# Optimization experiments

Hardware: AMD Instinct MI355X
Metric: run time of the kernel (lower is better)

Reference implementation:

```python
import jax, jax.numpy as jnp
import numpy as np

B, C, H, W = 16, 256, 64, 64
HEADS = 8


def setup_inputs() -> dict:
    key = jax.random.key(0)
    ks = jax.random.split(key, 12)
    s = 0.02
    return {
        "x": jax.random.normal(ks[0], (B, C, H, W), jnp.float32),
        "Wq": jax.random.normal(ks[1], (C, C), jnp.float32) * s,
        "bq": jnp.zeros((C,), jnp.float32),
        "Wk": jax.random.normal(ks[2], (C, C), jnp.float32) * s,
        "bk": jnp.zeros((C,), jnp.float32),
        "Wv": jax.random.normal(ks[3], (C, C), jnp.float32) * s,
        "bv": jnp.zeros((C,), jnp.float32),
        "gamma": jax.random.normal(ks[4], (1,), jnp.float32) * 0.5,
        "beta": jax.random.normal(ks[5], (1,), jnp.float32) * 0.5,
        "W1": jax.random.normal(ks[6], (C, C), jnp.float32) * s,
        "b1": jnp.zeros((C,), jnp.float32),
        "u1": jax.random.normal(ks[7], (C,), jnp.float32),
        "W2": jax.random.normal(ks[8], (C, C), jnp.float32) * s,
        "b2": jnp.zeros((C,), jnp.float32),
        "u2": jax.random.normal(ks[9], (C,), jnp.float32),
    }


def _conv1x1(x, Wt, b):
    # 1x1 conv == per-pixel GEMM over channels
    return jnp.einsum('oc,bchw->bohw', Wt, x) + b[None, :, None, None]


def _l2(v):
    return v / (jnp.linalg.norm(v) + 1e-12)


def _spectral_norm(Wt, u):
    # one power iteration (torch SpectralNorm wrapper), u treated as buffer
    Wm = Wt.reshape(Wt.shape[0], -1)
    v = _l2(Wm.T @ u)
    u_new = _l2(Wm @ v)
    sigma = u_new @ (Wm @ v)
    return Wt / sigma


def reference(x, Wq, bq, Wk, bk, Wv, bv, gamma, beta, W1, b1, u1, W2, b2, u2):
    Bn, Cn, Hh, Ww = x.shape
    N = Hh * Ww
    d = Cn // HEADS
    scale = HEADS ** (-0.5)
    # 1x1 conv projections, then b (h n) s layout -> (B, heads, d, N)
    q = _conv1x1(x, Wq, bq).reshape(Bn, HEADS, d, N)
    k = _conv1x1(x, Wk, bk).reshape(Bn, HEADS, d, N)
    v = _conv1x1(x, Wv, bv).reshape(Bn, HEADS, d, N)
    # per-head channel attention: energy is (B, heads, d, d)
    energy = jnp.einsum('bhis,bhjs->bhij', q, k) * scale
    attn = jax.nn.softmax(energy, axis=-1)
    out = jnp.einsum('bhij,bhjs->bhis', attn, v).reshape(Bn, Cn, Hh, Ww)
    out = gamma * out + x
    # residual refinement net (dropout = identity in eval mode)
    y = _conv1x1(out, _spectral_norm(W1, u1), b1)
    y = jax.nn.leaky_relu(y, 0.1)
    y = _conv1x1(y, _spectral_norm(W2, u2), b2)
    out = out + beta * y
    return (out, attn)
```

## Files before the change

kernel.cpp:

```cpp
#include <hip/hip_runtime.h>
#include <hip/hip_bf16.h>
#include <cstdint>
#include <cstddef>

typedef __attribute__((ext_vector_type(8))) __bf16 bf16x8;
typedef __attribute__((ext_vector_type(4))) float f32x4;
typedef __attribute__((ext_vector_type(8))) unsigned short us8;
typedef __attribute__((ext_vector_type(4))) unsigned short us4;

__device__ __forceinline__ unsigned short f2bf(float f){
  unsigned int u = __float_as_uint(f);
  u += 0x7fffu + ((u >> 16) & 1u);
  return (unsigned short)(u >> 16);
}
__device__ __forceinline__ float bf2f(unsigned short h){
  return __uint_as_float(((unsigned int)h) << 16);
}
__device__ __forceinline__ bf16x8 ldbf8(const unsigned short* p){
  return __builtin_bit_cast(bf16x8, *(const us8*)p);
}
__device__ __forceinline__ void split16(const float* __restrict__ g,
                                        unsigned short* __restrict__ hs,
                                        unsigned short* __restrict__ ls){
  #pragma unroll
  for (int q = 0; q < 4; ++q){
    float4 v = *(const float4*)(g + q*4);
    unsigned short h0=f2bf(v.x), h1=f2bf(v.y), h2=f2bf(v.z), h3=f2bf(v.w);
    us4 hv = {h0,h1,h2,h3};
    us4 lv = { f2bf(v.x - bf2f(h0)), f2bf(v.y - bf2f(h1)),
               f2bf(v.z - bf2f(h2)), f2bf(v.w - bf2f(h3)) };
    *(us4*)(hs + q*4) = hv;
    *(us4*)(ls + q*4) = lv;
  }
}

#define SCALE_E 0.35355339059327373f

static const size_t OFF_XHI    = 0;
static const size_t OFF_XLO    = 33554432;
static const size_t OFF_XTHI   = 67108864;
static const size_t OFF_GPART  = 100663296;
static const size_t OFF_G      = 113246208;
static const size_t OFF_M      = 117440512;
static const size_t OFF_W1S    = 119537664;
static const size_t OFF_W2S    = 119668736;
static const size_t OFF_SIG    = 119799808;
static const size_t OFF_XSUM   = 119799824;
static const size_t OFF_ROWADD = 119816208;

__global__ void k_zero(float* __restrict__ xsum){
  xsum[blockIdx.x * 256 + threadIdx.x] = 0.f;
}

__global__ void k_sigma(const float* __restrict__ W1, const float* __restrict__ u1,
                        const float* __restrict__ W2, const float* __restrict__ u2,
                        float* __restrict__ sig){
  const float* W = blockIdx.x ? W2 : W1;
  const float* u = blockIdx.x ? u2 : u1;
  int t = threadIdx.x;
  __shared__ __align__(16) float red[256];
  __shared__ __align__(16) float vls[256];
  __shared__ __align__(16) float uls[256];
  uls[t] = u[t];
  __syncthreads();
  float t1 = 0.f;
  for (int o = 0; o < 256; ++o) t1 += W[o*256 + t] * uls[o];
  red[t] = t1 * t1;
  __syncthreads();
  for (int s = 128; s > 0; s >>= 1){ if (t < s) red[t] += red[t+s]; __syncthreads(); }
  float nrm = sqrtf(red[0]);
  vls[t] = t1 / (nrm + 1e-12f);
  __syncthreads();
  float w = 0.f;
  const float4* wr4 = (const float4*)(W + t*256);
  for (int c4 = 0; c4 < 64; ++c4){
    float4 a = wr4[c4];
    float4 v = *(const float4*)&vls[c4*4];
    w += a.x*v.x + a.y*v.y + a.z*v.z + a.w*v.w;
  }
  __syncthreads();
  red[t] = w * w;
  __syncthreads();
  for (int s = 128; s > 0; s >>= 1){ if (t < s) red[t] += red[t+s]; __syncthreads(); }
  if (t == 0){
    float s2 = red[0];
    float sn = sqrtf(s2);
    sig[blockIdx.x] = s2 / (sn + 1e-12f);
  }
}

__global__ void k_wconv(const float* __restrict__ W1, const float* __restrict__ W2,
                        const float* __restrict__ sig,
                        unsigned short* __restrict__ W1s, unsigned short* __restrict__ W2s){
  int sel = blockIdx.x >> 6;
  const float* W = sel ? W2 : W1;
  unsigned short* o = sel ? W2s : W1s;
  float inv = 1.0f / sig[sel];
  int base = (blockIdx.x & 63) * 1024 + threadIdx.x * 4;
  float4 v = *(const float4*)&W[base];
  us4 r = { f2bf(v.x*inv), f2bf(v.y*inv), f2bf(v.z*inv), f2bf(v.w*inv) };
  *(us4*)&o[base] = r;
}

__global__ __launch_bounds__(256) void k_convert(const float* __restrict__ x,
    unsigned short* __restrict__ xhi, unsigned short* __restrict__ xlo,
    unsigned short* __restrict__ xthi, float* __restrict__ xsum){
  int b = blockIdx.z, c0 = blockIdx.y*64, n0 = blockIdx.x*64;
  int t = threadIdx.x, tn = t & 15, tc = t >> 4;
  __shared__ __align__(16) unsigned short hs[64][68];
  __shared__ __align__(16) float ps[64][17];
  #pragma unroll
  for (int rr = 0; rr < 4; ++rr){
    int cl = rr*16 + tc;
    size_t gro = ((size_t)(b*256 + c0 + cl))*4096 + n0 + tn*4;
    float4 v = *(const float4*)&x[gro];
    unsigned short h0=f2bf(v.x), h1=f2bf(v.y), h2=f2bf(v.z), h3=f2bf(v.w);
    us4 hv = {h0,h1,h2,h3};
    us4 lv = { f2bf(v.x - bf2f(h0)), f2bf(v.y - bf2f(h1)),
               f2bf(v.z - bf2f(h2)), f2bf(v.w - bf2f(h3)) };
    *(us4*)&xhi[gro] = hv;
    *(us4*)&xlo[gro] = lv;
    *(us4*)&hs[cl][tn*4] = hv;
    ps[cl][tn] = v.x + v.y + v.z + v.w;
  }
  __syncthreads();
  #pragma unroll
  for (int rr = 0; rr < 4; ++rr){
    int nl = rr*16 + tc;
    int cl4 = tn*4;
    us4 w = { hs[cl4+0][nl], hs[cl4+1][nl], hs[cl4+2][nl], hs[cl4+3][nl] };
    *(us4*)&xthi[((size_t)(b*4096 + n0 + nl))*256 + c0 + cl4] = w;
  }
  if (t < 64){
    float s = 0.f;
    #pragma unroll
    for (int k = 0; k < 16; ++k) s += ps[t][k];
    atomicAdd(&xsum[b*256 + c0 + t], s);
  }
}

__global__ __launch_bounds__(256) void k_gram(const unsigned short* __restrict__ xhi,
    const unsigned short* __restrict__ xlo, float* __restrict__ G, float* __restrict__ Gp){
  int b = blockIdx.z;
  int tr = (blockIdx.y >> 1) * 128, tc = (blockIdx.y & 1) * 128;
  int kc = blockIdx.x * 1024;
  int t = threadIdx.x;
  __shared__ __align__(16) unsigned short Ah[2][128*40], Al[2][128*40],
                                          Bh[2][128*40], Bl[2][128*40];
  f32x4 acc[4][4];
  #pragma unroll
  for (int i = 0; i < 4; ++i)
    #pragma unroll
    for (int j = 0; j < 4; ++j) acc[i][j] = (f32x4){0.f,0.f,0.f,0.f};
  int srow = t >> 1, skh = (t & 1) * 16;
  int l = t & 63, wv = t >> 6;
  int wr = (wv >> 1) * 64, wc = (wv & 1) * 64;
  int lr = l & 15, lg = l >> 4;
  size_t bb = (size_t)b * 256 * 4096;
  const unsigned short* gah = xhi + bb + (size_t)(tr + srow)*4096 + kc + skh;
  const unsigned short* gal = xlo + bb + (size_t)(tr + srow)*4096 + kc + skh;
  const unsigned short* gbh = xhi + bb + (size_t)(tc + srow)*4096 + kc + skh;
  const unsigned short* gbl = xlo + bb + (size_t)(tc + srow)*4096 + kc + skh;
  us8 rah0 = *(const us8*)gah, rah1 = *(const us8*)(gah + 8);
  us8 ral0 = *(const us8*)gal, ral1 = *(const us8*)(gal + 8);
  us8 rbh0 = *(const us8*)gbh, rbh1 = *(const us8*)(gbh + 8);
  us8 rbl0 = *(const us8*)gbl, rbl1 = *(const us8*)(gbl + 8);
  int cur = 0;
  for (int ki = 0; ki < 32; ++ki){
    *(us8*)&Ah[cur][srow*40 + skh]     = rah0;
    *(us8*)&Ah[cur][srow*40 + skh + 8] = rah1;
    *(us8*)&Al[cur][srow*40 + skh]     = ral0;
    *(us8*)&Al[cur][srow*40 + skh + 8] = ral1;
    *(us8*)&Bh[cur][srow*40 + skh]     = rbh0;
    *(us8*)&Bh[cur][srow*40 + skh + 8] = rbh1;
    *(us8*)&Bl[cur][srow*40 + skh]     = rbl0;
    *(us8*)&Bl[cur][srow*40 + skh + 8] = rbl1;
    if (ki < 31){
      int ko = (ki + 1) * 32;
      rah0 = *(const us8*)(gah + ko); rah1 = *(const us8*)(gah + ko + 8);
      ral0 = *(const us8*)(gal + ko); ral1 = *(const us8*)(gal + ko + 8);
      rbh0 = *(const us8*)(gbh + ko); rbh1 = *(const us8*)(gbh + ko + 8);
      rbl0 = *(const us8*)(gbl + ko); rbl1 = *(const us8*)(gbl + ko + 8);
    }
    __syncthreads();
    bf16x8 ah[4], alv[4], bh[4], blv[4];
    #pragma unroll
    for (int i = 0; i < 4; ++i){
      ah[i]  = ldbf8(&Ah[cur][(wr + i*16 + lr)*40 + lg*8]);
      alv[i] = ldbf8(&Al[cur][(wr + i*16 + lr)*40 + lg*8]);
      bh[i]  = ldbf8(&Bh[cur][(wc + i*16 + lr)*40 + lg*8]);
      blv[i] = ldbf8(&Bl[cur][(wc + i*16 + lr)*40 + lg*8]);
    }
    #pragma unroll
    for (int i = 0; i < 4; ++i)
      #pragma unroll
      for (int j = 0; j < 4; ++j){
        acc[i][j] = __builtin_amdgcn_mfma_f32_16x16x32_bf16(ah[i],  bh[j],  acc[i][j], 0,0,0);
        acc[i][j] = __builtin_amdgcn_mfma_f32_16x16x32_bf16(ah[i],  blv[j], acc[i][j], 0,0,0);
        acc[i][j] = __builtin_amdgcn_mfma_f32_16x16x32_bf16(alv[i], bh[j],  acc[i][j], 0,0,0);
      }
    cur ^= 1;
  }
  float* dst = (blockIdx.x == 0) ? (G + (size_t)b*65536)
                                 : (Gp + ((size_t)(blockIdx.x - 1)*16 + b)*65536);
  #pragma unroll
  for (int i = 0; i < 4; ++i)
    #pragma unroll
    for (int j = 0; j < 4; ++j)
      #pragma unroll
      for (int r = 0; r < 4; ++r){
        int row = tr + wr + i*16 + lg*4 + r;
        int col = tc + wc + j*16 + lr;
        dst[row*256 + col] = acc[i][j][r];
      }
}

__global__ void k_gred(const float* __restrict__ G0, const float* __restrict__ Gp,
                       unsigned short* __restrict__ Ghi, unsigned short* __restrict__ Glo){
  size_t idx = ((size_t)blockIdx.x * 256 + threadIdx.x) * 4;
  float4 g  = *(const float4*)&G0[idx];
  float4 p0 = *(const float4*)&Gp[idx];
  float4 p1 = *(const float4*)&Gp[idx + 1048576];
  float4 p2 = *(const float4*)&Gp[idx + 2097152];
  float s0 = g.x + p0.x + p1.x + p2.x;
  float s1 = g.y + p0.y + p1.y + p2.y;
  float s2 = g.z + p0.z + p1.z + p2.z;
  float s3 = g.w + p0.w + p1.w + p2.w;
  unsigned short h0=f2bf(s0), h1=f2bf(s1), h2=f2bf(s2), h3=f2bf(s3);
  us4 hv = {h0,h1,h2,h3};
  us4 lv = { f2bf(s0 - bf2f(h0)), f2bf(s1 - bf2f(h1)),
             f2bf(s2 - bf2f(h2)), f2bf(s3 - bf2f(h3)) };
  *(us4*)&Ghi[idx] = hv;
  *(us4*)&Glo[idx] = lv;
}

__global__ __launch_bounds__(256) void k_qg(const float* __restrict__ Wq,
    const unsigned short* __restrict__ Ghi, const unsigned short* __restrict__ Glo,
    unsigned short* __restrict__ Phi, unsigned short* __restrict__ Plo){
  int b = blockIdx.z;
  int tr = blockIdx.y * 128, tc = blockIdx.x * 128;
  int t = threadIdx.x;
  __shared__ __align__(16) unsigned short Ah[128*40], Al[128*40], Bh[128*40], Bl[128*40];
  f32x4 acc[4][4];
  #pragma unroll
  for (int i = 0; i < 4; ++i)
    #pragma unroll
    for (int j = 0; j < 4; ++j) acc[i][j] = (f32x4){0.f,0.f,0.f,0.f};
  int srow = t >> 1, skh = (t & 1) * 16;
  int l = t & 63, wv = t >> 6;
  int wr = (wv >> 1) * 64, wc = (wv & 1) * 64;
  int lr = l & 15, lg = l >> 4;
  for (int kk = 0; kk < 256; kk += 32){
    __syncthreads();
    split16(Wq + (size_t)(tr + srow)*256 + kk + skh, &Ah[srow*40 + skh], &Al[srow*40 + skh]);
    size_t gb = (size_t)b*65536 + (size_t)(tc + srow)*256 + kk + skh;
    *(us8*)&Bh[srow*40 + skh]     = *(const us8*)&Ghi[gb];
    *(us8*)&Bh[srow*40 + skh + 8] = *(const us8*)&Ghi[gb + 8];
    *(us8*)&Bl[srow*40 + skh]     = *(const us8*)&Glo[gb];
    *(us8*)&Bl[srow*40 + skh + 8] = *(const us8*)&Glo[gb + 8];
    __syncthreads();
    bf16x8 ah[4], alv[4], bh[4], blv[4];
    #pragma unroll
    for (int i = 0; i < 4; ++i){
      ah[i]  = ldbf8(&Ah[(wr + i*16 + lr)*40 + lg*8]);
      alv[i] = ldbf8(&Al[(wr + i*16 + lr)*40 + lg*8]);
      bh[i]  = ldbf8(&Bh[(wc + i*16 + lr)*40 + lg*8]);
      blv[i] = ldbf8(&Bl[(wc + i*16 + lr)*40 + lg*8]);
    }
    #pragma unroll
    for (int i = 0; i < 4; ++i)
      #pragma unroll
      for (int j = 0; j < 4; ++j){
        acc[i][j] = __builtin_amdgcn_mfma_f32_16x16x32_bf16(ah[i],  bh[j],  acc[i][j], 0,0,0);
        acc[i][j] = __builtin_amdgcn_mfma_f32_16x16x32_bf16(ah[i],  blv[j], acc[i][j], 0,0,0);
        acc[i][j] = __builtin_amdgcn_mfma_f32_16x16x32_bf16(alv[i], bh[j],  acc[i][j], 0,0,0);
      }
  }
  #pragma unroll
  for (int i = 0; i < 4; ++i)
    #pragma unroll
    for (int j = 0; j < 4; ++j)
      #pragma unroll
      for (int r = 0; r < 4; ++r){
        int row = tr + wr + i*16 + lg*4 + r;
        int col = tc + wc + j*16 + lr;
        size_t off = (size_t)b*65536 + (size_t)row*256 + col;
        float p = acc[i][j][r];
        unsigned short hp = f2bf(p);
        Phi[off] = hp;
        Plo[off] = f2bf(p - bf2f(hp));
      }
}

__global__ __launch_bounds__(256) void k_e(const unsigned short* __restrict__ Phi,
    const unsigned short* __restrict__ Plo, const float* __restrict__ Wk,
    float* __restrict__ Ef){
  int b = blockIdx.z;
  int tr = blockIdx.y * 128, tc = blockIdx.x * 128;
  int t = threadIdx.x;
  __shared__ __align__(16) unsigned short Ah[128*40], Al[128*40], Bh[128*40], Bl[128*40];
  f32x4 acc[4][4];
  #pragma unroll
  for (int i = 0; i < 4; ++i)
    #pragma unroll
    for (int j = 0; j < 4; ++j) acc[i][j] = (f32x4){0.f,0.f,0.f,0.f};
  int srow = t >> 1, skh = (t & 1) * 16;
  int l = t & 63, wv = t >> 6;
  int wr = (wv >> 1) * 64, wc = (wv & 1) * 64;
  int lr = l & 15, lg = l >> 4;
  for (int kk = 0; kk < 256; kk += 32){
    __syncthreads();
    size_t ga = (size_t)b*65536 + (size_t)(tr + srow)*256 + kk + skh;
    *(us8*)&Ah[srow*40 + skh]     = *(const us8*)&Phi[ga];
    *(us8*)&Ah[srow*40 + skh + 8] = *(const us8*)&Phi[ga + 8];
    *(us8*)&Al[srow*40 + skh]     = *(const us8*)&Plo[ga];
    *(us8*)&Al[srow*40 + skh + 8] = *(const us8*)&Plo[ga + 8];
    split16(Wk + (size_t)(tc + srow)*256 + kk + skh, &Bh[srow*40 + skh], &Bl[srow*40 + skh]);
    __syncthreads();
    bf16x8 ah[4], alv[4], bh[4], blv[4];
    #pragma unroll
    for (int i = 0; i < 4; ++i){
      ah[i]  = ldbf8(&Ah[(wr + i*16 + lr)*40 + lg*8]);
      alv[i] = ldbf8(&Al[(wr + i*16 + lr)*40 + lg*8]);
      bh[i]  = ldbf8(&Bh[(wc + i*16 + lr)*40 + lg*8]);
      blv[i] = ldbf8(&Bl[(wc + i*16 + lr)*40 + lg*8]);
    }
    #pragma unroll
    for (int i = 0; i < 4; ++i)
      #pragma unroll
      for (int j = 0; j < 4; ++j){
        acc[i][j] = __builtin_amdgcn_mfma_f32_16x16x32_bf16(ah[i],  bh[j],  acc[i][j], 0,0,0);
        acc[i][j] = __builtin_amdgcn_mfma_f32_16x16x32_bf16(ah[i],  blv[j], acc[i][j], 0,0,0);
        acc[i][j] = __builtin_amdgcn_mfma_f32_16x16x32_bf16(alv[i], bh[j],  acc[i][j], 0,0,0);
      }
  }
  #pragma unroll
  for (int i = 0; i < 4; ++i)
    #pragma unroll
    for (int j = 0; j < 4; ++j)
      #pragma unroll
      for (int r = 0; r < 4; ++r){
        int row = tr + wr + i*16 + lg*4 + r;
        int col = tc + wc + j*16 + lr;
        Ef[(size_t)b*65536 + (size_t)row*256 + col] = SCALE_E * acc[i][j][r];
      }
}

__global__ __launch_bounds__(256) void k_soft(const float* __restrict__ Ef,
    const float* __restrict__ Wq, const float* __restrict__ bq,
    const float* __restrict__ Wk, const float* __restrict__ bk,
    const float* __restrict__ Wv, const float* __restrict__ bv,
    const float* __restrict__ gptr, const float* __restrict__ xsum,
    unsigned short* __restrict__ Mw, float* __restrict__ rowadd,
    float* __restrict__ attn_out){
  int blk = blockIdx.x, b = blk >> 3, h = blk & 7;
  int t = threadIdx.x;
  int i = t >> 3, j4 = (t & 7) * 4;
  __shared__ __align__(16) float Aw[32][40];
  __shared__ float qsv[32], ksv[32];
  if (t < 64){
    int r = t & 31;
    const float* Wm = (t < 32) ? Wq : Wk;
    const float4* wr4 = (const float4*)(Wm + (size_t)(h*32 + r)*256);
    const float4* xs4 = (const float4*)(xsum + b*256);
    float s = 0.f;
    #pragma unroll
    for (int c4 = 0; c4 < 64; ++c4){
      float4 a = wr4[c4], xv = xs4[c4];
      s += a.x*xv.x + a.y*xv.y + a.z*xv.z + a.w*xv.w;
    }
    if (t < 32) qsv[r] = s; else ksv[r] = s;
  }
  __syncthreads();
  float4 e = *(const float4*)&Ef[(size_t)b*65536 + (size_t)(h*32 + i)*256 + h*32 + j4];
  float bqi = bq[h*32 + i];
  float qb  = qsv[i] + 4096.f * bqi;
  e.x += SCALE_E * (bqi*ksv[j4+0] + bk[h*32+j4+0]*qb);
  e.y += SCALE_E * (bqi*ksv[j4+1] + bk[h*32+j4+1]*qb);
  e.z += SCALE_E * (bqi*ksv[j4+2] + bk[h*32+j4+2]*qb);
  e.w += SCALE_E * (bqi*ksv[j4+3] + bk[h*32+j4+3]*qb);
  float m = fmaxf(fmaxf(e.x, e.y), fmaxf(e.z, e.w));
  m = fmaxf(m, __shfl_xor(m, 1));
  m = fmaxf(m, __shfl_xor(m, 2));
  m = fmaxf(m, __shfl_xor(m, 4));
  float ex0 = expf(e.x - m), ex1 = expf(e.y - m), ex2 = expf(e.z - m), ex3 = expf(e.w - m);
  float s = ex0 + ex1 + ex2 + ex3;
  s += __shfl_xor(s, 1); s += __shfl_xor(s, 2); s += __shfl_xor(s, 4);
  float inv = 1.f / s;
  float4 a4 = { ex0*inv, ex1*inv, ex2*inv, ex3*inv };
  *(float4*)&attn_out[(((size_t)(b*8 + h))*32 + i)*32 + j4] = a4;
  *(float4*)&Aw[i][j4] = a4;
  __syncthreads();
  float gamma = gptr[0];
  float mr[32];
  #pragma unroll
  for (int r = 0; r < 32; ++r) mr[r] = 0.f;
  for (int j = 0; j < 32; ++j){
    float wvv = Wv[(size_t)(h*32 + j)*256 + t];
    #pragma unroll
    for (int r = 0; r < 32; ++r) mr[r] += Aw[r][j] * wvv;
  }
  unsigned short* Mrow = Mw + ((size_t)b*256 + h*32)*256 + t;
  #pragma unroll
  for (int r = 0; r < 32; ++r){
    float diag = (h*32 + r == t) ? 1.f : 0.f;
    Mrow[r*256] = f2bf(gamma * mr[r] + diag);
  }
  if (t < 32){
    float sr = 0.f;
    #pragma unroll
    for (int j = 0; j < 32; ++j) sr += Aw[t][j] * bv[h*32 + j];
    rowadd[b*256 + h*32 + t] = gamma * sr;
  }
}

template<int MODE>
__global__ __launch_bounds__(256) void k_gemm(const unsigned short* __restrict__ Aall,
    const unsigned short* __restrict__ Bmat, const unsigned short* __restrict__ oth,
    const float* __restrict__ rowadd, const float* __restrict__ bias,
    const float* __restrict__ betap,
    unsigned short* __restrict__ outb){
  int b = blockIdx.z;
  int n0 = blockIdx.x * 128, o0 = blockIdx.y * 128;
  int t = threadIdx.x;
  __shared__ __align__(16) unsigned short Als[2][128*40], Bls[2][128*40];
  f32x4 acc[4][4];
  #pragma unroll
  for (int i = 0; i < 4; ++i)
    #pragma unroll
    for (int j = 0; j < 4; ++j) acc[i][j] = (f32x4){0.f,0.f,0.f,0.f};
  const unsigned short* A  = Aall + (size_t)b * 1048576;
  const unsigned short* Bp = (MODE == 0) ? (Bmat + (size_t)b * 65536) : Bmat;
  int srow = t >> 1, skh = (t & 1) * 16;
  int l = t & 63, wv = t >> 6;
  int wr = (wv >> 1) * 64, wc = (wv & 1) * 64;
  int lr = l & 15, lg = l >> 4;
  const unsigned short* ga = A  + (size_t)(n0 + srow)*256 + skh;
  const unsigned short* gb = Bp + (size_t)(o0 + srow)*256 + skh;
  us8 ra0 = *(const us8*)ga, ra1 = *(const us8*)(ga + 8);
  us8 rb0 = *(const us8*)gb, rb1 = *(const us8*)(gb + 8);
  #pragma unroll
  for (int ki = 0; ki < 8; ++ki){
    int cur = ki & 1;
    *(us8*)&Als[cur][srow*40 + skh]     = ra0;
    *(us8*)&Als[cur][srow*40 + skh + 8] = ra1;
    *(us8*)&Bls[cur][srow*40 + skh]     = rb0;
    *(us8*)&Bls[cur][srow*40 + skh + 8] = rb1;
    if (ki < 7){
      int ko = (ki + 1) * 32;
      ra0 = *(const us8*)(ga + ko); ra1 = *(const us8*)(ga + ko + 8);
      rb0 = *(const us8*)(gb + ko); rb1 = *(const us8*)(gb + ko + 8);
    }
    __syncthreads();
    bf16x8 af[4], bfv[4];
    #pragma unroll
    for (int i = 0; i < 4; ++i) af[i]  = ldbf8(&Als[cur][(wr + i*16 + lr)*40 + lg*8]);
    #pragma unroll
    for (int j = 0; j < 4; ++j) bfv[j] = ldbf8(&Bls[cur][(wc + j*16 + lr)*40 + lg*8]);
    #pragma unroll
    for (int i = 0; i < 4; ++i)
      #pragma unroll
      for (int j = 0; j < 4; ++j)
        acc[i][j] = __builtin_amdgcn_mfma_f32_16x16x32_bf16(af[i], bfv[j], acc[i][j], 0,0,0);
  }
  float beta = (MODE == 2) ? betap[0] : 0.f;
  #pragma unroll
  for (int j = 0; j < 4; ++j){
    int oc = o0 + wc + j*16 + lr;
    float bvl = (MODE == 0) ? rowadd[b*256 + oc] : bias[oc];
    #pragma unroll
    for (int i = 0; i < 4; ++i){
      #pragma unroll
      for (int r = 0; r < 4; ++r){
        int n = n0 + wr + i*16 + lg*4 + r;
        size_t off = ((size_t)b*4096 + n)*256 + oc;
        float v = acc[i][j][r];
        if (MODE == 0){
          v += bvl;
          outb[off] = f2bf(v);
        } else if (MODE == 1){
          v += bvl;
          v = (v > 0.f) ? v : 0.1f * v;
          outb[off] = f2bf(v);
        } else {
          v = bf2f(oth[off]) + beta * (v + bvl);
          outb[off] = f2bf(v);
        }
      }
    }
  }
}

__global__ __launch_bounds__(256) void k_tpose(const unsigned short* __restrict__ fin,
                                               float* __restrict__ out){
  int b = blockIdx.z, c0 = blockIdx.y*64, n0 = blockIdx.x*64;
  int t = threadIdx.x, tn = t & 15, tc = t >> 4;
  __shared__ __align__(16) unsigned short ts[64][68];
  #pragma unroll
  for (int rr = 0; rr < 4; ++rr){
    int nl = rr*16 + tc;
    us4 v = *(const us4*)&fin[((size_t)(b*4096 + n0 + nl))*256 + c0 + tn*4];
    *(us4*)&ts[nl][tn*4] = v;
  }
  __syncthreads();
  #pragma unroll
  for (int rr = 0; rr < 4; ++rr){
    int cl = rr*16 + tc;
    int nl4 = tn*4;
    float4 v = { bf2f(ts[nl4+0][cl]), bf2f(ts[nl4+1][cl]),
                 bf2f(ts[nl4+2][cl]), bf2f(ts[nl4+3][cl]) };
    *(float4*)&out[((size_t)(b*256 + c0 + cl))*4096 + n0 + nl4] = v;
  }
}

extern "C" void kernel_launch(void* const* d_in, const int* in_sizes, int n_in,
                              void* d_out, int out_size, void* d_ws, size_t ws_size,
                              hipStream_t stream){
  const float* x    = (const float*)d_in[0];
  const float* Wq   = (const float*)d_in[1];
  const float* bq   = (const float*)d_in[2];
  const float* Wk   = (const float*)d_in[3];
  const float* bk   = (const float*)d_in[4];
  const float* Wv   = (const float*)d_in[5];
  const float* bv   = (const float*)d_in[6];
  const float* gamma= (const float*)d_in[7];
  const float* beta = (const float*)d_in[8];
  const float* W1   = (const float*)d_in[9];
  const float* b1   = (const float*)d_in[10];
  const float* u1   = (const float*)d_in[11];
  const float* W2   = (const float*)d_in[12];
  const float* b2   = (const float*)d_in[13];
  const float* u2   = (const float*)d_in[14];

  char* ws = (char*)d_ws;
  unsigned short* xhi   = (unsigned short*)(ws + OFF_XHI);
  unsigned short* xlo   = (unsigned short*)(ws + OFF_XLO);
  unsigned short* xthi  = (unsigned short*)(ws + OFF_XTHI);
  float*          Gp    = (float*)(ws + OFF_GPART);
  float*          G0    = (float*)(ws + OFF_G);
  unsigned short* Mw    = (unsigned short*)(ws + OFF_M);
  unsigned short* W1s   = (unsigned short*)(ws + OFF_W1S);
  unsigned short* W2s   = (unsigned short*)(ws + OFF_W2S);
  float*          sig   = (float*)(ws + OFF_SIG);
  float*          xsum  = (float*)(ws + OFF_XSUM);
  float*          rowadd= (float*)(ws + OFF_ROWADD);
  unsigned short* Ghi   = (unsigned short*)(ws + OFF_XLO);
  unsigned short* Glo   = (unsigned short*)(ws + OFF_XLO + 2097152);
  unsigned short* Phi   = (unsigned short*)(ws + OFF_GPART);
  unsigned short* Plo   = (unsigned short*)(ws + OFF_GPART + 2097152);
  float*          Ef    = (float*)(ws + OFF_GPART + 4194304);
  unsigned short* othi  = xlo;
  unsigned short* y1t   = xhi;
  unsigned short* finT  = xthi;

  float* outF  = (float*)d_out;
  float* attnO = outF + 16777216;

  k_zero<<<dim3(16), dim3(256), 0, stream>>>(xsum);
  k_sigma<<<dim3(2), dim3(256), 0, stream>>>(W1, u1, W2, u2, sig);
  k_wconv<<<dim3(128), dim3(256), 0, stream>>>(W1, W2, sig, W1s, W2s);
  k_convert<<<dim3(64,4,16), dim3(256), 0, stream>>>(x, xhi, xlo, xthi, xsum);
  k_gram<<<dim3(4,4,16), dim3(256), 0, stream>>>(xhi, xlo, G0, Gp);
  k_gred<<<dim3(1024), dim3(256), 0, stream>>>(G0, Gp, Ghi, Glo);
  k_qg<<<dim3(2,2,16), dim3(256), 0, stream>>>(Wq, Ghi, Glo, Phi, Plo);
  k_e<<<dim3(2,2,16), dim3(256), 0, stream>>>(Phi, Plo, Wk, Ef);
  k_soft<<<dim3(128), dim3(256), 0, stream>>>(Ef, Wq, bq, Wk, bk, Wv, bv,
                                              gamma, xsum, Mw, rowadd, attnO);
  k_gemm<0><<<dim3(32,2,16), dim3(256), 0, stream>>>(xthi, Mw, othi, rowadd, b1, beta, othi);
  k_gemm<1><<<dim3(32,2,16), dim3(256), 0, stream>>>(othi, W1s, othi, rowadd, b1, beta, y1t);
  k_gemm<2><<<dim3(32,2,16), dim3(256), 0, stream>>>(y1t, W2s, othi, rowadd, b2, beta, finT);
  k_tpose<<<dim3(64,4,16), dim3(256), 0, stream>>>(finT, outF);
}
```

Baseline: 371.8 us.

## Use direct global-to-LDS loads with XOR-swizzled tiles in gram and GEMM kernels

Replaces the register-staged global loads followed by LDS stores with global_load_lds (16-byte) direct-to-LDS transfers in the gram and GEMM kernels. The padded 40-element row stride is replaced by an unpadded 32-element stride with an XOR swizzle to limit bank conflicts. The barrier moves to the end of each k-step. This is meant to cut VGPR pressure and LDS store instructions and to overlap the next tile's load with MFMA work. The risk is that the swizzle mapping or the wait/barrier ordering is wrong, and that the direct loads are not waited on before the barrier.

```diff
diff --git a/kernel.cpp b/kernel.cpp
--- a/kernel.cpp
+++ b/kernel.cpp
@@ -18,6 +18,11 @@
 }
 __device__ __forceinline__ bf16x8 ldbf8(const unsigned short* p){
   return __builtin_bit_cast(bf16x8, *(const us8*)p);
+}
+__device__ __forceinline__ void gload_lds16(const unsigned short* g, unsigned short* l){
+  __builtin_amdgcn_global_load_lds(
+      (__attribute__((address_space(1))) void*)(g),
+      (__attribute__((address_space(3))) void*)(l), 16, 0, 0);
 }
 __device__ __forceinline__ void split16(const float* __restrict__ g,
                                         unsigned short* __restrict__ hs,
@@ -145,51 +150,47 @@
   int tr = (blockIdx.y >> 1) * 128, tc = (blockIdx.y & 1) * 128;
   int kc = blockIdx.x * 1024;
   int t = threadIdx.x;
-  __shared__ __align__(16) unsigned short Ah[2][128*40], Al[2][128*40],
-                                          Bh[2][128*40], Bl[2][128*40];
+  __shared__ __align__(16) unsigned short Ah[2][4096], Al[2][4096],
+                                          Bh[2][4096], Bl[2][4096];
   f32x4 acc[4][4];
   #pragma unroll
   for (int i = 0; i < 4; ++i)
     #pragma unroll
     for (int j = 0; j < 4; ++j) acc[i][j] = (f32x4){0.f,0.f,0.f,0.f};
-  int srow = t >> 1, skh = (t & 1) * 16;
-  int l = t & 63, wv = t >> 6;
-  int wr = (wv >> 1) * 64, wc = (wv & 1) * 64;
+  int w = t >> 6, lane = t & 63;
+  int srw = lane >> 2;
+  int csw = ((lane & 3) ^ ((lane >> 3) & 3)) * 8;
+  int l = t & 63;
+  int wr = (w >> 1) * 64, wc = (w & 1) * 64;
   int lr = l & 15, lg = l >> 4;
+  int swz = (lr >> 1) & 3;
   size_t bb = (size_t)b * 256 * 4096;
-  const unsigned short* gah = xhi + bb + (size_t)(tr + srow)*4096 + kc + skh;
-  const unsigned short* gal = xlo + bb + (size_t)(tr + srow)*4096 + kc + skh;
-  const unsigned short* gbh = xhi + bb + (size_t)(tc + srow)*4096 + kc + skh;
-  const unsigned short* gbl = xlo + bb + (size_t)(tc + srow)*4096 + kc + skh;
-  us8 rah0 = *(const us8*)gah, rah1 = *(const us8*)(gah + 8);
-  us8 ral0 = *(const us8*)gal, ral1 = *(const us8*)(gal + 8);
-  us8 rbh0 = *(const us8*)gbh, rbh1 = *(const us8*)(gbh + 8);
-  us8 rbl0 = *(const us8*)gbl, rbl1 = *(const us8*)(gbl + 8);
-  int cur = 0;
+  auto STAGE = [&](int buf, int kk){
+    #pragma unroll
+    for (int j = 0; j < 2; ++j){
+      int row = w*32 + j*16;
+      size_t gra = bb + (size_t)(tr + row + srw)*4096 + kk + csw;
+      size_t grb = bb + (size_t)(tc + row + srw)*4096 + kk + csw;
+      gload_lds16(xhi + gra, &Ah[buf][row*32]);
+      gload_lds16(xlo + gra, &Al[buf][row*32]);
+      gload_lds16(xhi + grb, &Bh[buf][row*32]);
+      gload_lds16(xlo + grb, &Bl[buf][row*32]);
+    }
+  };
+  STAGE(0, kc);
+  __syncthreads();
   for (int ki = 0; ki < 32; ++ki){
-    *(us8*)&Ah[cur][srow*40 + skh]     = rah0;
-    *(us8*)&Ah[cur][srow*40 + skh + 8] = rah1;
-    *(us8*)&Al[cur][srow*40 + skh]     = ral0;
-    *(us8*)&Al[cur][srow*40 + skh + 8] = ral1;
-    *(us8*)&Bh[cur][srow*40 + skh]     = rbh0;
-    *(us8*)&Bh[cur][srow*40 + skh + 8] = rbh1;
-    *(us8*)&Bl[cur][srow*40 + skh]     = rbl0;
-    *(us8*)&Bl[cur][srow*40 + skh + 8] = rbl1;
-    if (ki < 31){
-      int ko = (ki + 1) * 32;
-      rah0 = *(const us8*)(gah + ko); rah1 = *(const us8*)(gah + ko + 8);
-      ral0 = *(const us8*)(gal + ko); ral1 = *(const us8*)(gal + ko + 8);
-      rbh0 = *(const us8*)(gbh + ko); rbh1 = *(const us8*)(gbh + ko + 8);
-      rbl0 = *(const us8*)(gbl + ko); rbl1 = *(const us8*)(gbl + ko + 8);
-    }
-    __syncthreads();
+    int cur = ki & 1;
+    if (ki < 31) STAGE(cur ^ 1, kc + (ki + 1) * 32);
     bf16x8 ah[4], alv[4], bh[4], blv[4];
     #pragma unroll
     for (int i = 0; i < 4; ++i){
-      ah[i]  = ldbf8(&Ah[cur][(wr + i*16 + lr)*40 + lg*8]);
-      alv[i] = ldbf8(&Al[cur][(wr + i*16 + lr)*40 + lg*8]);
-      bh[i]  = ldbf8(&Bh[cur][(wc + i*16 + lr)*40 + lg*8]);
-      blv[i] = ldbf8(&Bl[cur][(wc + i*16 + lr)*40 + lg*8]);
+      int ra = (wr + i*16 + lr)*32 + ((lg ^ swz) * 8);
+      int rb = (wc + i*16 + lr)*32 + ((lg ^ swz) * 8);
+      ah[i]  = ldbf8(&Ah[cur][ra]);
+      alv[i] = ldbf8(&Al[cur][ra]);
+      bh[i]  = ldbf8(&Bh[cur][rb]);
+      blv[i] = ldbf8(&Bl[cur][rb]);
     }
     #pragma unroll
     for (int i = 0; i < 4; ++i)
@@ -199,7 +200,7 @@
         acc[i][j] = __builtin_amdgcn_mfma_f32_16x16x32_bf16(ah[i],  blv[j], acc[i][j], 0,0,0);
         acc[i][j] = __builtin_amdgcn_mfma_f32_16x16x32_bf16(alv[i], bh[j],  acc[i][j], 0,0,0);
       }
-    cur ^= 1;
+    __syncthreads();
   }
   float* dst = (blockIdx.x == 0) ? (G + (size_t)b*65536)
                                  : (Gp + ((size_t)(blockIdx.x - 1)*16 + b)*65536);
@@ -423,7 +424,7 @@
   int b = blockIdx.z;
   int n0 = blockIdx.x * 128, o0 = blockIdx.y * 128;
   int t = threadIdx.x;
-  __shared__ __align__(16) unsigned short Als[2][128*40], Bls[2][128*40];
+  __shared__ __align__(16) unsigned short Als[2][4096], Bls[2][4096];
   f32x4 acc[4][4];
   #pragma unroll
   for (int i = 0; i < 4; ++i)
@@ -431,37 +432,39 @@
     for (int j = 0; j < 4; ++j) acc[i][j] = (f32x4){0.f,0.f,0.f,0.f};
   const unsigned short* A  = Aall + (size_t)b * 1048576;
   const unsigned short* Bp = (MODE == 0) ? (Bmat + (size_t)b * 65536) : Bmat;
-  int srow = t >> 1, skh = (t & 1) * 16;
-  int l = t & 63, wv = t >> 6;
-  int wr = (wv >> 1) * 64, wc = (wv & 1) * 64;
+  int w = t >> 6, lane = t & 63;
+  int srw = lane >> 2;
+  int csw = ((lane & 3) ^ ((lane >> 3) & 3)) * 8;
+  int l = t & 63;
+  int wr = (w >> 1) * 64, wc = (w & 1) * 64;
   int lr = l & 15, lg = l >> 4;
-  const unsigned short* ga = A  + (size_t)(n0 + srow)*256 + skh;
-  const unsigned short* gb = Bp + (size_t)(o0 + srow)*256 + skh;
-  us8 ra0 = *(const us8*)ga, ra1 = *(const us8*)(ga + 8);
-  us8 rb0 = *(const us8*)gb, rb1 = *(const us8*)(gb + 8);
+  int swz = (lr >> 1) & 3;
+  auto STAGE = [&](int buf, int kk){
+    #pragma unroll
+    for (int j = 0; j < 2; ++j){
+      int row = w*32 + j*16;
+      gload_lds16(A  + (size_t)(n0 + row + srw)*256 + kk + csw, &Als[buf][row*32]);
+      gload_lds16(Bp + (size_t)(o0 + row + srw)*256 + kk + csw, &Bls[buf][row*32]);
+    }
+  };
+  STAGE(0, 0);
+  __syncthreads();
   #pragma unroll
   for (int ki = 0; ki < 8; ++ki){
     int cur = ki & 1;
-    *(us8*)&Als[cur][srow*40 + skh]     = ra0;
-    *(us8*)&Als[cur][srow*40 + skh + 8] = ra1;
-    *(us8*)&Bls[cur][srow*40 + skh]     = rb0;
-    *(us8*)&Bls[cur][srow*40 + skh + 8] = rb1;
-    if (ki < 7){
-      int ko = (ki + 1) * 32;
-      ra0 = *(const us8*)(ga + ko); ra1 = *(const us8*)(ga + ko + 8);
-      rb0 = *(const us8*)(gb + ko); rb1 = *(const us8*)(gb + ko + 8);
-    }
-    __syncthreads();
+    if (ki < 7) STAGE(cur ^ 1, (ki + 1) * 32);
     bf16x8 af[4], bfv[4];
     #pragma unroll
-    for (int i = 0; i < 4; ++i) af[i]  = ldbf8(&Als[cur][(wr + i*16 + lr)*40 + lg*8]);
-    #pragma unroll
-    for (int j = 0; j < 4; ++j) bfv[j] = ldbf8(&Bls[cur][(wc + j*16 + lr)*40 + lg*8]);
+    for (int i = 0; i < 4; ++i){
+      af[i]  = ldbf8(&Als[cur][(wr + i*16 + lr)*32 + ((lg ^ swz) * 8)]);
+      bfv[i] = ldbf8(&Bls[cur][(wc + i*16 + lr)*32 + ((lg ^ swz) * 8)]);
+    }
     #pragma unroll
     for (int i = 0; i < 4; ++i)
       #pragma unroll
       for (int j = 0; j < 4; ++j)
         acc[i][j] = __builtin_amdgcn_mfma_f32_16x16x32_bf16(af[i], bfv[j], acc[i][j], 0,0,0);
+    __syncthreads();
   }
   float beta = (MODE == 2) ? betap[0] : 0.f;
   #pragma unroll
```

Result: no change. 373.1 us (+0.4%).
